# Kernel tuning notes

Measured on AMD Instinct MI355X. Metric: run time of the kernel, lower is better.

Reference implementation:

```python
import jax, jax.numpy as jnp
import numpy as np

NP, NO, E, IN_DIM, D = 100000, 200000, 500000, 512, 256
EPS = 1e-12  # torch F.normalize default eps


def setup_inputs() -> dict:
    key = jax.random.key(0)
    ks = jax.random.split(key, 12)
    return {
        "feat_prefix": jax.random.normal(ks[0], (NP, IN_DIM), jnp.float32),
        "feat_other": jax.random.normal(ks[1], (NO, IN_DIM), jnp.float32),
        "src": jax.random.randint(ks[2], (E,), 0, NP),
        "dst": jax.random.randint(ks[3], (E,), 0, NO),
        "Wm_p": jax.random.normal(ks[4], (IN_DIM, D), jnp.float32) * 0.02,
        "bm_p": jax.random.normal(ks[5], (D,), jnp.float32) * 0.02,
        "Wm_o": jax.random.normal(ks[6], (IN_DIM, D), jnp.float32) * 0.02,
        "bm_o": jax.random.normal(ks[7], (D,), jnp.float32) * 0.02,
        "W": jax.random.normal(ks[8], (D, D), jnp.float32) * 0.02,
        "bW": jax.random.normal(ks[9], (D,), jnp.float32) * 0.02,
        "a_w": jax.random.normal(ks[10], (2 * D,), jnp.float32) * 0.02,
        "a_b": jax.random.normal(ks[11], (1,), jnp.float32) * 0.02,
    }


def _l2norm(x):
    n = jnp.linalg.norm(x, axis=-1, keepdims=True)
    return x / jnp.maximum(n, EPS)


def reference(feat_prefix, feat_other, src, dst,
              Wm_p, bm_p, Wm_o, bm_o, W, bW, a_w, a_b):
    # FeatureMappingLayer: per-ntype Linear + ReLU
    hp = jax.nn.relu(feat_prefix @ Wm_p + bm_p)   # [NP, D]
    ho = jax.nn.relu(feat_other @ Wm_o + bm_o)    # [NO, D]
    d = hp.shape[1]
    n_prefix = hp.shape[0]

    # GAT-style score: a([W h_src ; W h_dst]) -- project at node level,
    # decompose the concat-linear into two per-node dot products, then gather.
    hp_proj = hp @ W + bW                         # [NP, D]
    ho_proj = ho @ W + bW                         # [NO, D]
    s_src = hp_proj @ a_w[:d]                     # [NP]
    s_dst = ho_proj @ a_w[d:]                     # [NO]
    e = s_src[src] + s_dst[dst] + a_b[0]          # [E] per-edge scores

    # Segment softmax over source (Prefix) node
    m = jax.ops.segment_max(e, src, num_segments=n_prefix)
    m = jnp.where(jnp.isfinite(m), m, 0.0)        # empty segments -> 0
    ex = jnp.exp(e - m[src])
    denom = jax.ops.segment_sum(ex, src, num_segments=n_prefix)
    alpha = ex / denom[src]                       # [E]

    # Scatter-weighted sum of mapped (pre-W) dst features into Prefix nodes
    agg = jax.ops.segment_sum(alpha[:, None] * ho[dst], src,
                              num_segments=n_prefix)  # [NP, D]

    return (_l2norm(agg), _l2norm(ho))
```

## Files before the change

### kernel.cpp

```cpp
#include <hip/hip_runtime.h>
#include <math.h>

#define IN_DIM 512
#define DD 256
#define NEG_INF -3.402823466e+38f

typedef __attribute__((ext_vector_type(8))) short short8_t;
typedef __attribute__((ext_vector_type(4))) float f32x4_t;

__device__ __forceinline__ void split1(float x, ushort& h, ushort& l) {
  unsigned u = __float_as_uint(x);
  unsigned hr = (u + 0x7FFFu + ((u >> 16) & 1u)) >> 16;
  h = (ushort)hr;
  float hf = __uint_as_float(hr << 16);
  float lf = x - hf;
  l = (ushort)(__float_as_uint(lf) >> 16);
}

__device__ __forceinline__ void split8(const float4& a, const float4& b,
                                       short8_t& h, short8_t& l) {
  ushort hh, ll;
  split1(a.x, hh, ll); h[0] = (short)hh; l[0] = (short)ll;
  split1(a.y, hh, ll); h[1] = (short)hh; l[1] = (short)ll;
  split1(a.z, hh, ll); h[2] = (short)hh; l[2] = (short)ll;
  split1(a.w, hh, ll); h[3] = (short)hh; l[3] = (short)ll;
  split1(b.x, hh, ll); h[4] = (short)hh; l[4] = (short)ll;
  split1(b.y, hh, ll); h[5] = (short)hh; l[5] = (short)ll;
  split1(b.z, hh, ll); h[6] = (short)hh; l[6] = (short)ll;
  split1(b.w, hh, ll); h[7] = (short)hh; l[7] = (short)ll;
}

__global__ void prep_w2(const float* __restrict__ W, const float* __restrict__ a_w,
                        float* __restrict__ w2) {
  int i = threadIdx.x;
  float s = 0.f;
  for (int j = 0; j < DD; ++j) s = fmaf(W[i * DD + j], a_w[DD + j], s);
  w2[i] = s;
}

__global__ void bsplit_kernel(const float* __restrict__ Wm,
                              ushort* __restrict__ Bh, ushort* __restrict__ Bl) {
  int i = blockIdx.x * 256 + threadIdx.x;
  int k = i >> 8, col = i & 255;
  float x = Wm[i];
  unsigned u = __float_as_uint(x);
  unsigned hr = (u + 0x7FFFu + ((u >> 16) & 1u)) >> 16;
  float hf = __uint_as_float(hr << 16);
  float lf = x - hf;
  unsigned ul = __float_as_uint(lf);
  ushort l = (ushort)((ul + 0x7FFFu + ((ul >> 16) & 1u)) >> 16);
  int kc16 = k >> 5, kr = k & 31;
  int lane = ((kr >> 3) << 4) | (col & 15);
  int nf = col >> 4;
  int off = (((((kc16 << 4) + nf) << 6) + lane) << 3) + (kr & 7);
  Bh[off] = (ushort)hr;
  Bl[off] = l;
}

__global__ __launch_bounds__(256, 2) void map_gemm_mfma(
    const float* __restrict__ X, const ushort* __restrict__ Bh,
    const ushort* __restrict__ Bl, const float* __restrict__ bm,
    const float* __restrict__ w2, float* __restrict__ Yn,
    float* __restrict__ tvals, float* __restrict__ wnorm, int M) {
  __shared__ ushort Ah[2][4096];
  __shared__ ushort Al[2][4096];
  const int t = threadIdx.x;
  const int w = t >> 6;
  const int l = t & 63;
  const int c = l & 15;
  const int g = l >> 4;
  const int row0 = blockIdx.x * 64;

  const int sr = t >> 2;
  const int skb = (t & 3) << 4;
  int gr = row0 + sr;
  if (gr >= M) gr = M - 1;
  const float* xrow = X + (size_t)gr * IN_DIM;

  f32x4_t acc[4][4];
#pragma unroll
  for (int m = 0; m < 4; ++m)
#pragma unroll
    for (int n = 0; n < 4; ++n) acc[m][n] = (f32x4_t){0.f, 0.f, 0.f, 0.f};

  const int sw = (sr & 7) << 3;
  const int i0 = ((sr << 6) + skb);
  const short8_t* bhb = reinterpret_cast<const short8_t*>(Bh);
  const short8_t* blb = reinterpret_cast<const short8_t*>(Bl);

  float4 r0, r1, r2, r3;
  {
    const float4* p = reinterpret_cast<const float4*>(xrow + skb);
    r0 = p[0]; r1 = p[1]; r2 = p[2]; r3 = p[3];
    short8_t h0, h1, l0, l1;
    split8(r0, r1, h0, l0);
    split8(r2, r3, h1, l1);
    *reinterpret_cast<short8_t*>(&Ah[0][i0 ^ sw]) = h0;
    *reinterpret_cast<short8_t*>(&Ah[0][(i0 + 8) ^ sw]) = h1;
    *reinterpret_cast<short8_t*>(&Al[0][i0 ^ sw]) = l0;
    *reinterpret_cast<short8_t*>(&Al[0][(i0 + 8) ^ sw]) = l1;
  }
  __syncthreads();

  for (int ks = 0; ks < 8; ++ks) {
    const int cur = ks & 1;
    if (ks < 7) {
      const float4* p = reinterpret_cast<const float4*>(xrow + ((ks + 1) << 6) + skb);
      r0 = p[0]; r1 = p[1]; r2 = p[2]; r3 = p[3];
    }

#pragma unroll
    for (int kc = 0; kc < 2; ++kc) {
      const int kc16 = (ks << 1) + kc;
      short8_t ah[4], av[4];
#pragma unroll
      for (int m = 0; m < 4; ++m) {
        int r = (m << 4) + c;
        int idx = ((r << 6) + (kc << 5) + (g << 3)) ^ ((r & 7) << 3);
        ah[m] = *reinterpret_cast<const short8_t*>(&Ah[cur][idx]);
        av[m] = *reinterpret_cast<const short8_t*>(&Al[cur][idx]);
      }
      short8_t bh[4], bl[4];
#pragma unroll
      for (int n = 0; n < 4; ++n) {
        const int boff = (((kc16 << 4) + (w << 2) + n) << 6) + l;
        bh[n] = bhb[boff];
        bl[n] = blb[boff];
      }
#pragma unroll
      for (int n = 0; n < 4; ++n)
#pragma unroll
        for (int m = 0; m < 4; ++m) {
          acc[m][n] = __builtin_amdgcn_mfma_f32_16x16x32_bf16(ah[m], bh[n], acc[m][n], 0, 0, 0);
          acc[m][n] = __builtin_amdgcn_mfma_f32_16x16x32_bf16(ah[m], bl[n], acc[m][n], 0, 0, 0);
          acc[m][n] = __builtin_amdgcn_mfma_f32_16x16x32_bf16(av[m], bh[n], acc[m][n], 0, 0, 0);
        }
    }

    if (ks < 7) {
      short8_t h0, h1, l0, l1;
      split8(r0, r1, h0, l0);
      split8(r2, r3, h1, l1);
      const int nxt = cur ^ 1;
      *reinterpret_cast<short8_t*>(&Ah[nxt][i0 ^ sw]) = h0;
      *reinterpret_cast<short8_t*>(&Ah[nxt][(i0 + 8) ^ sw]) = h1;
      *reinterpret_cast<short8_t*>(&Al[nxt][i0 ^ sw]) = l0;
      *reinterpret_cast<short8_t*>(&Al[nxt][(i0 + 8) ^ sw]) = l1;
    }
    __syncthreads();
  }

  float bv[4], wv[4];
#pragma unroll
  for (int n = 0; n < 4; ++n) {
    bv[n] = bm[(w << 6) + (n << 4) + c];
    wv[n] = w2[(w << 6) + (n << 4) + c];
  }
#pragma unroll
  for (int m = 0; m < 4; ++m)
#pragma unroll
    for (int n = 0; n < 4; ++n)
#pragma unroll
      for (int q = 0; q < 4; ++q) {
        float v = acc[m][n][q] + bv[n];
        acc[m][n][q] = v > 0.f ? v : 0.f;
      }

  float* red = reinterpret_cast<float*>(&Ah[0][0]);
  float pss[4][4], pdt[4][4];
#pragma unroll
  for (int m = 0; m < 4; ++m)
#pragma unroll
    for (int q = 0; q < 4; ++q) {
      float ss = 0.f, dt = 0.f;
#pragma unroll
      for (int n = 0; n < 4; ++n) {
        float a = acc[m][n][q];
        ss = fmaf(a, a, ss);
        dt = fmaf(a, wv[n], dt);
      }
      for (int d = 8; d; d >>= 1) {
        ss += __shfl_down(ss, d, 16);
        dt += __shfl_down(dt, d, 16);
      }
      pss[m][q] = ss;
      pdt[m][q] = dt;
    }
  __syncthreads();
#pragma unroll
  for (int m = 0; m < 4; ++m)
#pragma unroll
    for (int q = 0; q < 4; ++q)
      if (c == 0) {
        int rr = (m << 4) + (g << 2) + q;
        red[(w << 6) + rr] = pss[m][q];
        red[256 + (w << 6) + rr] = pdt[m][q];
      }
  __syncthreads();
  if (t < 64) {
    float ss = red[t] + red[64 + t] + red[128 + t] + red[192 + t];
    float dt = red[256 + t] + red[320 + t] + red[384 + t] + red[448 + t];
    float nr = sqrtf(ss);
    red[512 + t] = 1.f / fmaxf(nr, 1e-12f);
    int r = row0 + t;
    if (r < M) {
      float tv = expf(dt);
      tvals[r] = tv;
      wnorm[r] = tv * nr;
    }
  }
  __syncthreads();
#pragma unroll
  for (int m = 0; m < 4; ++m)
#pragma unroll
    for (int q = 0; q < 4; ++q) {
      int rr = (m << 4) + (g << 2) + q;
      float sc = red[512 + rr];
      int r = row0 + rr;
      if (r < M) {
#pragma unroll
        for (int n = 0; n < 4; ++n)
          Yn[(size_t)r * DD + (w << 6) + (n << 4) + c] = acc[m][n][q] * sc;
      }
    }
}

__global__ void hist_kernel(const int* __restrict__ src, int* __restrict__ deg, int E) {
  int i = blockIdx.x * blockDim.x + threadIdx.x;
  if (i < E) atomicAdd(&deg[src[i]], 1);
}

__global__ __launch_bounds__(256) void scan_part(const int* __restrict__ deg,
                                                 int* __restrict__ bsum, int NP) {
  __shared__ int s[256];
  int t = threadIdx.x, b = blockIdx.x;
  int i0 = (b * 256 + t) * 2;
  int v0 = (i0 < NP) ? deg[i0] : 0;
  int v1 = (i0 + 1 < NP) ? deg[i0 + 1] : 0;
  s[t] = v0 + v1;
  __syncthreads();
  for (int off = 128; off; off >>= 1) {
    if (t < off) s[t] += s[t + off];
    __syncthreads();
  }
  if (t == 0) bsum[b] = s[0];
}

__global__ __launch_bounds__(256) void scan_top(int* __restrict__ bsum,
                                                int* __restrict__ rowptr_last) {
  __shared__ int s[256];
  int t = threadIdx.x;
  int v = bsum[t];
  s[t] = v;
  __syncthreads();
  for (int off = 1; off < 256; off <<= 1) {
    int u = (t >= off) ? s[t - off] : 0;
    __syncthreads();
    s[t] += u;
    __syncthreads();
  }
  bsum[t] = s[t] - v;
  if (t == 255) *rowptr_last = s[255];
}

__global__ __launch_bounds__(256) void scan_fin(const int* __restrict__ deg,
                                                const int* __restrict__ bsum,
                                                int* __restrict__ rowptr,
                                                int* __restrict__ cursor, int NP) {
  __shared__ int s[256];
  int t = threadIdx.x, b = blockIdx.x;
  int i0 = (b * 256 + t) * 2;
  int v0 = (i0 < NP) ? deg[i0] : 0;
  int v1 = (i0 + 1 < NP) ? deg[i0 + 1] : 0;
  int local = v0 + v1;
  s[t] = local;
  __syncthreads();
  for (int off = 1; off < 256; off <<= 1) {
    int u = (t >= off) ? s[t - off] : 0;
    __syncthreads();
    s[t] += u;
    __syncthreads();
  }
  int base = bsum[b] + s[t] - local;
  if (i0 < NP) { rowptr[i0] = base; cursor[i0] = base; }
  if (i0 + 1 < NP) { rowptr[i0 + 1] = base + v0; cursor[i0 + 1] = base + v0; }
}

__global__ void fill_kernel(const int* __restrict__ src, const int* __restrict__ dst,
                            int* __restrict__ cursor, int* __restrict__ ebuf, int E) {
  int i = blockIdx.x * blockDim.x + threadIdx.x;
  if (i < E) {
    int pos = atomicAdd(&cursor[src[i]], 1);
    ebuf[pos] = dst[i];
  }
}

__global__ void agg_kernel(const int* __restrict__ rowptr, const int* __restrict__ ebuf,
                           const float* __restrict__ tvals, const float* __restrict__ wnorm,
                           const float* __restrict__ hon, float* __restrict__ agg, int NP) {
  int p = (int)(((long)blockIdx.x * blockDim.x + threadIdx.x) >> 6);
  int lane = threadIdx.x & 63;
  if (p >= NP) return;
  int beg = rowptr[p], end = rowptr[p + 1];
  float4 acc = {0.f, 0.f, 0.f, 0.f};
  if (beg < end) {
    float den = 0.f;
    for (int j = beg + lane; j < end; j += 64) den += tvals[ebuf[j]];
#pragma unroll
    for (int d = 32; d > 0; d >>= 1) den += __shfl_xor(den, d, 64);
    float inv = 1.f / den;
    int d0 = ebuf[beg];
    float wcur = wnorm[d0];
    float4 v = *reinterpret_cast<const float4*>(&hon[(size_t)d0 * DD + lane * 4]);
    for (int j = beg + 1; j <= end; ++j) {
      float4 vn = {0.f, 0.f, 0.f, 0.f};
      float wnext = 0.f;
      if (j < end) {
        int dn = ebuf[j];
        wnext = wnorm[dn];
        vn = *reinterpret_cast<const float4*>(&hon[(size_t)dn * DD + lane * 4]);
      }
      float wa = wcur * inv;
      acc.x = fmaf(wa, v.x, acc.x);
      acc.y = fmaf(wa, v.y, acc.y);
      acc.z = fmaf(wa, v.z, acc.z);
      acc.w = fmaf(wa, v.w, acc.w);
      v = vn; wcur = wnext;
    }
  }
  float ss = acc.x * acc.x + acc.y * acc.y + acc.z * acc.z + acc.w * acc.w;
#pragma unroll
  for (int d = 32; d > 0; d >>= 1) ss += __shfl_xor(ss, d, 64);
  float inv = 1.0f / fmaxf(sqrtf(ss), 1e-12f);
  float4 o = {acc.x * inv, acc.y * inv, acc.z * inv, acc.w * inv};
  *reinterpret_cast<float4*>(&agg[(size_t)p * DD + lane * 4]) = o;
}

extern "C" void kernel_launch(void* const* d_in, const int* in_sizes, int n_in,
                              void* d_out, int out_size, void* d_ws, size_t ws_size,
                              hipStream_t stream) {
  const float* feat_other = (const float*)d_in[1];
  const int* src = (const int*)d_in[2];
  const int* dst = (const int*)d_in[3];
  const float* Wm_o = (const float*)d_in[6];
  const float* bm_o = (const float*)d_in[7];
  const float* W = (const float*)d_in[8];
  const float* a_w = (const float*)d_in[10];

  const int NP = in_sizes[0] / IN_DIM;
  const int NO = in_sizes[1] / IN_DIM;
  const int E = in_sizes[2];

  float* out = (float*)d_out;
  float* agg_out = out;
  float* ho_out = out + (size_t)NP * DD;

  float* ws = (float*)d_ws;
  float* tvals = ws;
  float* wnorm = tvals + NO;
  float* w2 = wnorm + NO;
  int* deg = (int*)(w2 + 256);
  int* rowptr = deg + NP;
  int* cursor = rowptr + NP + 1;
  int* bsum = cursor + NP;
  int* ebuf = bsum + 256;
  size_t foff = (size_t)(2 * NO) + 256 + NP + (NP + 1) + NP + 256 + E;
  foff = (foff + 3) & ~(size_t)3;
  ushort* Bh = (ushort*)(ws + foff);
  ushort* Bl = Bh + (size_t)IN_DIM * DD;

  hipMemsetAsync(deg, 0, (size_t)NP * sizeof(int), stream);

  prep_w2<<<1, 256, 0, stream>>>(W, a_w, w2);
  bsplit_kernel<<<(IN_DIM * DD) / 256, 256, 0, stream>>>(Wm_o, Bh, Bl);

  map_gemm_mfma<<<(NO + 63) / 64, 256, 0, stream>>>(
      feat_other, Bh, Bl, bm_o, w2, ho_out, tvals, wnorm, NO);

  hist_kernel<<<(E + 255) / 256, 256, 0, stream>>>(src, deg, E);
  scan_part<<<256, 256, 0, stream>>>(deg, bsum, NP);
  scan_top<<<1, 256, 0, stream>>>(bsum, rowptr + NP);
  scan_fin<<<256, 256, 0, stream>>>(deg, bsum, rowptr, cursor, NP);
  fill_kernel<<<(E + 255) / 256, 256, 0, stream>>>(src, dst, cursor, ebuf, E);

  agg_kernel<<<(NP * 64 + 255) / 256, 256, 0, stream>>>(
      rowptr, ebuf, tvals, wnorm, ho_out, agg_out, NP);
}
```

Baseline: 401.7 us.

## Use single-pass fp16 MFMA, drop softmax denominator, deepen agg prefetch

```diff
diff --git a/kernel.cpp b/kernel.cpp
--- a/kernel.cpp
+++ b/kernel.cpp
@@ -3,32 +3,9 @@
 
 #define IN_DIM 512
 #define DD 256
-#define NEG_INF -3.402823466e+38f
-
-typedef __attribute__((ext_vector_type(8))) short short8_t;
+
+typedef _Float16 half8_t __attribute__((ext_vector_type(8)));
 typedef __attribute__((ext_vector_type(4))) float f32x4_t;
-
-__device__ __forceinline__ void split1(float x, ushort& h, ushort& l) {
-  unsigned u = __float_as_uint(x);
-  unsigned hr = (u + 0x7FFFu + ((u >> 16) & 1u)) >> 16;
-  h = (ushort)hr;
-  float hf = __uint_as_float(hr << 16);
-  float lf = x - hf;
-  l = (ushort)(__float_as_uint(lf) >> 16);
-}
-
-__device__ __forceinline__ void split8(const float4& a, const float4& b,
-                                       short8_t& h, short8_t& l) {
-  ushort hh, ll;
-  split1(a.x, hh, ll); h[0] = (short)hh; l[0] = (short)ll;
-  split1(a.y, hh, ll); h[1] = (short)hh; l[1] = (short)ll;
-  split1(a.z, hh, ll); h[2] = (short)hh; l[2] = (short)ll;
-  split1(a.w, hh, ll); h[3] = (short)hh; l[3] = (short)ll;
-  split1(b.x, hh, ll); h[4] = (short)hh; l[4] = (short)ll;
-  split1(b.y, hh, ll); h[5] = (short)hh; l[5] = (short)ll;
-  split1(b.z, hh, ll); h[6] = (short)hh; l[6] = (short)ll;
-  split1(b.w, hh, ll); h[7] = (short)hh; l[7] = (short)ll;
-}
 
 __global__ void prep_w2(const float* __restrict__ W, const float* __restrict__ a_w,
                         float* __restrict__ w2) {
@@ -38,32 +15,28 @@
   w2[i] = s;
 }
 
-__global__ void bsplit_kernel(const float* __restrict__ Wm,
-                              ushort* __restrict__ Bh, ushort* __restrict__ Bl) {
+__global__ void bconv_kernel(const float* __restrict__ Wm, _Float16* __restrict__ Bh) {
   int i = blockIdx.x * 256 + threadIdx.x;
   int k = i >> 8, col = i & 255;
-  float x = Wm[i];
-  unsigned u = __float_as_uint(x);
-  unsigned hr = (u + 0x7FFFu + ((u >> 16) & 1u)) >> 16;
-  float hf = __uint_as_float(hr << 16);
-  float lf = x - hf;
-  unsigned ul = __float_as_uint(lf);
-  ushort l = (ushort)((ul + 0x7FFFu + ((ul >> 16) & 1u)) >> 16);
   int kc16 = k >> 5, kr = k & 31;
   int lane = ((kr >> 3) << 4) | (col & 15);
   int nf = col >> 4;
   int off = (((((kc16 << 4) + nf) << 6) + lane) << 3) + (kr & 7);
-  Bh[off] = (ushort)hr;
-  Bl[off] = l;
+  Bh[off] = (_Float16)Wm[i];
+}
+
+__device__ __forceinline__ half8_t cvt8(const float4& a, const float4& b) {
+  half8_t h;
+  h[0] = (_Float16)a.x; h[1] = (_Float16)a.y; h[2] = (_Float16)a.z; h[3] = (_Float16)a.w;
+  h[4] = (_Float16)b.x; h[5] = (_Float16)b.y; h[6] = (_Float16)b.z; h[7] = (_Float16)b.w;
+  return h;
 }
 
 __global__ __launch_bounds__(256, 2) void map_gemm_mfma(
-    const float* __restrict__ X, const ushort* __restrict__ Bh,
-    const ushort* __restrict__ Bl, const float* __restrict__ bm,
-    const float* __restrict__ w2, float* __restrict__ Yn,
-    float* __restrict__ tvals, float* __restrict__ wnorm, int M) {
-  __shared__ ushort Ah[2][4096];
-  __shared__ ushort Al[2][4096];
+    const float* __restrict__ X, const _Float16* __restrict__ Bh,
+    const float* __restrict__ bm, const float* __restrict__ w2,
+    float* __restrict__ Yn, float* __restrict__ wnorm, int M) {
+  __shared__ ushort Ah[2][8192];
   const int t = threadIdx.x;
   const int w = t >> 6;
   const int l = t & 63;
@@ -72,7 +45,7 @@
   const int row0 = blockIdx.x * 64;
 
   const int sr = t >> 2;
-  const int skb = (t & 3) << 4;
+  const int skb = (t & 3) << 5;
   int gr = row0 + sr;
   if (gr >= M) gr = M - 1;
   const float* xrow = X + (size_t)gr * IN_DIM;
@@ -83,69 +56,57 @@
 #pragma unroll
     for (int n = 0; n < 4; ++n) acc[m][n] = (f32x4_t){0.f, 0.f, 0.f, 0.f};
 
-  const int sw = (sr & 7) << 3;
-  const int i0 = ((sr << 6) + skb);
-  const short8_t* bhb = reinterpret_cast<const short8_t*>(Bh);
-  const short8_t* blb = reinterpret_cast<const short8_t*>(Bl);
-
-  float4 r0, r1, r2, r3;
+  const int sw = (sr & 15) << 3;
+  const int i0 = (sr << 7) + skb;
+  const half8_t* bhb = reinterpret_cast<const half8_t*>(Bh);
+
+  float4 r0, r1, r2, r3, r4, r5, r6, r7;
   {
     const float4* p = reinterpret_cast<const float4*>(xrow + skb);
     r0 = p[0]; r1 = p[1]; r2 = p[2]; r3 = p[3];
-    short8_t h0, h1, l0, l1;
-    split8(r0, r1, h0, l0);
-    split8(r2, r3, h1, l1);
-    *reinterpret_cast<short8_t*>(&Ah[0][i0 ^ sw]) = h0;
-    *reinterpret_cast<short8_t*>(&Ah[0][(i0 + 8) ^ sw]) = h1;
-    *reinterpret_cast<short8_t*>(&Al[0][i0 ^ sw]) = l0;
-    *reinterpret_cast<short8_t*>(&Al[0][(i0 + 8) ^ sw]) = l1;
-  }
-  __syncthreads();
-
-  for (int ks = 0; ks < 8; ++ks) {
+    r4 = p[4]; r5 = p[5]; r6 = p[6]; r7 = p[7];
+    *reinterpret_cast<half8_t*>(&Ah[0][(i0 + 0) ^ sw]) = cvt8(r0, r1);
+    *reinterpret_cast<half8_t*>(&Ah[0][(i0 + 8) ^ sw]) = cvt8(r2, r3);
+    *reinterpret_cast<half8_t*>(&Ah[0][(i0 + 16) ^ sw]) = cvt8(r4, r5);
+    *reinterpret_cast<half8_t*>(&Ah[0][(i0 + 24) ^ sw]) = cvt8(r6, r7);
+  }
+  __syncthreads();
+
+  for (int ks = 0; ks < 4; ++ks) {
     const int cur = ks & 1;
-    if (ks < 7) {
-      const float4* p = reinterpret_cast<const float4*>(xrow + ((ks + 1) << 6) + skb);
+    if (ks < 3) {
+      const float4* p = reinterpret_cast<const float4*>(xrow + ((ks + 1) << 7) + skb);
       r0 = p[0]; r1 = p[1]; r2 = p[2]; r3 = p[3];
-    }
-
-#pragma unroll
-    for (int kc = 0; kc < 2; ++kc) {
-      const int kc16 = (ks << 1) + kc;
-      short8_t ah[4], av[4];
+      r4 = p[4]; r5 = p[5]; r6 = p[6]; r7 = p[7];
+    }
+
+#pragma unroll
+    for (int kc = 0; kc < 4; ++kc) {
+      const int kc16 = (ks << 2) + kc;
+      half8_t ah[4];
 #pragma unroll
       for (int m = 0; m < 4; ++m) {
         int r = (m << 4) + c;
-        int idx = ((r << 6) + (kc << 5) + (g << 3)) ^ ((r & 7) << 3);
-        ah[m] = *reinterpret_cast<const short8_t*>(&Ah[cur][idx]);
-        av[m] = *reinterpret_cast<const short8_t*>(&Al[cur][idx]);
-      }
-      short8_t bh[4], bl[4];
-#pragma unroll
-      for (int n = 0; n < 4; ++n) {
-        const int boff = (((kc16 << 4) + (w << 2) + n) << 6) + l;
-        bh[n] = bhb[boff];
-        bl[n] = blb[boff];
-      }
+        int idx = ((r << 7) + (kc << 5) + (g << 3)) ^ (c << 3);
+        ah[m] = *reinterpret_cast<const half8_t*>(&Ah[cur][idx]);
+      }
+      half8_t bh[4];
 #pragma unroll
       for (int n = 0; n < 4; ++n)
-#pragma unroll
-        for (int m = 0; m < 4; ++m) {
-          acc[m][n] = __builtin_amdgcn_mfma_f32_16x16x32_bf16(ah[m], bh[n], acc[m][n], 0, 0, 0);
-          acc[m][n] = __builtin_amdgcn_mfma_f32_16x16x32_bf16(ah[m], bl[n], acc[m][n], 0, 0, 0);
-          acc[m][n] = __builtin_amdgcn_mfma_f32_16x16x32_bf16(av[m], bh[n], acc[m][n], 0, 0, 0);
-        }
-    }
-
-    if (ks < 7) {
-      short8_t h0, h1, l0, l1;
-      split8(r0, r1, h0, l0);
-      split8(r2, r3, h1, l1);
+        bh[n] = bhb[(((kc16 << 4) + (w << 2) + n) << 6) + l];
+#pragma unroll
+      for (int n = 0; n < 4; ++n)
+#pragma unroll
+        for (int m = 0; m < 4; ++m)
+          acc[m][n] = __builtin_amdgcn_mfma_f32_16x16x32_f16(ah[m], bh[n], acc[m][n], 0, 0, 0);
+    }
+
+    if (ks < 3) {
       const int nxt = cur ^ 1;
-      *reinterpret_cast<short8_t*>(&Ah[nxt][i0 ^ sw]) = h0;
-      *reinterpret_cast<short8_t*>(&Ah[nxt][(i0 + 8) ^ sw]) = h1;
-      *reinterpret_cast<short8_t*>(&Al[nxt][i0 ^ sw]) = l0;
-      *reinterpret_cast<short8_t*>(&Al[nxt][(i0 + 8) ^ sw]) = l1;
+      *reinterpret_cast<half8_t*>(&Ah[nxt][(i0 + 0) ^ sw]) = cvt8(r0, r1);
+      *reinterpret_cast<half8_t*>(&Ah[nxt][(i0 + 8) ^ sw]) = cvt8(r2, r3);
+      *reinterpret_cast<half8_t*>(&Ah[nxt][(i0 + 16) ^ sw]) = cvt8(r4, r5);
+      *reinterpret_cast<half8_t*>(&Ah[nxt][(i0 + 24) ^ sw]) = cvt8(r6, r7);
     }
     __syncthreads();
   }
@@ -203,11 +164,7 @@
     float nr = sqrtf(ss);
     red[512 + t] = 1.f / fmaxf(nr, 1e-12f);
     int r = row0 + t;
-    if (r < M) {
-      float tv = expf(dt);
-      tvals[r] = tv;
-      wnorm[r] = tv * nr;
-    }
+    if (r < M) wnorm[r] = expf(dt) * nr;
   }
   __syncthreads();
 #pragma unroll
@@ -296,36 +253,37 @@
 }
 
 __global__ void agg_kernel(const int* __restrict__ rowptr, const int* __restrict__ ebuf,
-                           const float* __restrict__ tvals, const float* __restrict__ wnorm,
-                           const float* __restrict__ hon, float* __restrict__ agg, int NP) {
+                           const float* __restrict__ wnorm, const float* __restrict__ hon,
+                           float* __restrict__ agg, int NP) {
   int p = (int)(((long)blockIdx.x * blockDim.x + threadIdx.x) >> 6);
   int lane = threadIdx.x & 63;
   if (p >= NP) return;
   int beg = rowptr[p], end = rowptr[p + 1];
   float4 acc = {0.f, 0.f, 0.f, 0.f};
   if (beg < end) {
-    float den = 0.f;
-    for (int j = beg + lane; j < end; j += 64) den += tvals[ebuf[j]];
-#pragma unroll
-    for (int d = 32; d > 0; d >>= 1) den += __shfl_xor(den, d, 64);
-    float inv = 1.f / den;
     int d0 = ebuf[beg];
-    float wcur = wnorm[d0];
-    float4 v = *reinterpret_cast<const float4*>(&hon[(size_t)d0 * DD + lane * 4]);
-    for (int j = beg + 1; j <= end; ++j) {
+    float w0 = wnorm[d0];
+    float4 v0 = *reinterpret_cast<const float4*>(&hon[(size_t)d0 * DD + lane * 4]);
+    float w1 = 0.f;
+    float4 v1 = {0.f, 0.f, 0.f, 0.f};
+    if (beg + 1 < end) {
+      int d1 = ebuf[beg + 1];
+      w1 = wnorm[d1];
+      v1 = *reinterpret_cast<const float4*>(&hon[(size_t)d1 * DD + lane * 4]);
+    }
+    for (int j = beg; j < end; ++j) {
+      float wn_ = 0.f;
       float4 vn = {0.f, 0.f, 0.f, 0.f};
-      float wnext = 0.f;
-      if (j < end) {
-        int dn = ebuf[j];
-        wnext = wnorm[dn];
+      if (j + 2 < end) {
+        int dn = ebuf[j + 2];
+        wn_ = wnorm[dn];
         vn = *reinterpret_cast<const float4*>(&hon[(size_t)dn * DD + lane * 4]);
       }
-      float wa = wcur * inv;
-      acc.x = fmaf(wa, v.x, acc.x);
-      acc.y = fmaf(wa, v.y, acc.y);
-      acc.z = fmaf(wa, v.z, acc.z);
-      acc.w = fmaf(wa, v.w, acc.w);
-      v = vn; wcur = wnext;
+      acc.x = fmaf(w0, v0.x, acc.x);
+      acc.y = fmaf(w0, v0.y, acc.y);
+      acc.z = fmaf(w0, v0.z, acc.z);
+      acc.w = fmaf(w0, v0.w, acc.w);
+      w0 = w1; v0 = v1; w1 = wn_; v1 = vn;
     }
   }
   float ss = acc.x * acc.x + acc.y * acc.y + acc.z * acc.z + acc.w * acc.w;
@@ -356,26 +314,24 @@
   float* ho_out = out + (size_t)NP * DD;
 
   float* ws = (float*)d_ws;
-  float* tvals = ws;
-  float* wnorm = tvals + NO;
+  float* wnorm = ws;
   float* w2 = wnorm + NO;
   int* deg = (int*)(w2 + 256);
   int* rowptr = deg + NP;
   int* cursor = rowptr + NP + 1;
   int* bsum = cursor + NP;
   int* ebuf = bsum + 256;
-  size_t foff = (size_t)(2 * NO) + 256 + NP + (NP + 1) + NP + 256 + E;
+  size_t foff = (size_t)NO + 256 + NP + (NP + 1) + NP + 256 + E;
   foff = (foff + 3) & ~(size_t)3;
-  ushort* Bh = (ushort*)(ws + foff);
-  ushort* Bl = Bh + (size_t)IN_DIM * DD;
+  _Float16* Bh = (_Float16*)(ws + foff);
 
   hipMemsetAsync(deg, 0, (size_t)NP * sizeof(int), stream);
 
   prep_w2<<<1, 256, 0, stream>>>(W, a_w, w2);
-  bsplit_kernel<<<(IN_DIM * DD) / 256, 256, 0, stream>>>(Wm_o, Bh, Bl);
+  bconv_kernel<<<(IN_DIM * DD) / 256, 256, 0, stream>>>(Wm_o, Bh);
 
   map_gemm_mfma<<<(NO + 63) / 64, 256, 0, stream>>>(
-      feat_other, Bh, Bl, bm_o, w2, ho_out, tvals, wnorm, NO);
+      feat_other, Bh, bm_o, w2, ho_out, wnorm, NO);
 
   hist_kernel<<<(E + 255) / 256, 256, 0, stream>>>(src, deg, E);
   scan_part<<<256, 256, 0, stream>>>(deg, bsum, NP);
@@ -384,5 +340,5 @@
   fill_kernel<<<(E + 255) / 256, 256, 0, stream>>>(src, dst, cursor, ebuf, E);
 
   agg_kernel<<<(NP * 64 + 255) / 256, 256, 0, stream>>>(
-      rowptr, ebuf, tvals, wnorm, ho_out, agg_out, NP);
-}
+      rowptr, ebuf, wnorm, ho_out, agg_out, NP);
+}
```

After: 385.9 us. -3.9%, faster.
